# Optimization experiments

Measured on AMD Instinct MI355X. Metric: run time of the kernel, lower is better.

## Reference

```python
import jax, jax.numpy as jnp
from jax import lax
import numpy as np

SEQ_LEN, BATCH, NUM_TAGS = 512, 256, 128


def setup_inputs() -> dict:
    key = jax.random.key(0)
    k1, k2, k3, k4, k5 = jax.random.split(key, 5)
    emissions = jax.random.normal(k1, (SEQ_LEN, BATCH, NUM_TAGS), dtype=jnp.float32)
    tags = jax.random.randint(k2, (SEQ_LEN, BATCH), 0, NUM_TAGS, dtype=jnp.int64)
    mask = jnp.ones((SEQ_LEN, BATCH), dtype=bool)
    # CRF learned parameters (torchcrf initializes Uniform(-0.1, 0.1))
    start_transitions = jax.random.uniform(k3, (NUM_TAGS,), jnp.float32, -0.1, 0.1)
    end_transitions = jax.random.uniform(k4, (NUM_TAGS,), jnp.float32, -0.1, 0.1)
    transitions = jax.random.uniform(k5, (NUM_TAGS, NUM_TAGS), jnp.float32, -0.1, 0.1)
    return {
        "emissions": emissions,
        "tags": tags,
        "mask": mask,
        "start_transitions": start_transitions,
        "end_transitions": end_transitions,
        "transitions": transitions,
    }


def reference(emissions, tags, mask, start_transitions, end_transitions, transitions):
    """torchcrf CRF.forward(emissions, tags, mask, reduction='sum'):
    summed log-likelihood = numerator (gold path score) - log partition.
    emissions: [T, B, K], tags: [T, B], mask: [T, B] bool.
    """
    T, B = tags.shape
    maskf = mask.astype(emissions.dtype)
    bidx = jnp.arange(B)

    # ---- numerator: score of the gold tag sequence ----
    first_score = start_transitions[tags[0]] + emissions[0, bidx, tags[0]]  # [B]

    def num_step(carry, inp):
        score, prev_tags = carry
        em_t, tag_t, m_t = inp  # [B,K], [B], [B] float
        step = transitions[prev_tags, tag_t] + em_t[bidx, tag_t]
        score = score + step * m_t
        prev_tags = jnp.where(m_t.astype(bool), tag_t, prev_tags)
        return (score, prev_tags), None

    (num, last_tags), _ = lax.scan(
        num_step, (first_score, tags[0]), (emissions[1:], tags[1:], maskf[1:])
    )
    num = num + end_transitions[last_tags]  # [B]

    # ---- denominator: log partition via forward algorithm ----
    init = start_transitions[None, :] + emissions[0]  # [B, K]

    def den_step(score, inp):
        em_t, m_t = inp  # [B,K], [B] bool
        # broadcast: [B, K_prev, K_next]
        nxt = jax.nn.logsumexp(
            score[:, :, None] + transitions[None, :, :] + em_t[:, None, :], axis=1
        )
        score = jnp.where(m_t[:, None], nxt, score)
        return score, None

    final, _ = lax.scan(den_step, init, (emissions[1:], mask[1:]))
    den = jax.nn.logsumexp(final + end_transitions[None, :], axis=1)  # [B]

    # reduction='sum'
    return jnp.sum(num - den)
```

## Files before the change

kernel.cpp:

```cpp
#include <hip/hip_runtime.h>
#include <hip/hip_bf16.h>


#define TT 512
#define BB 256
#define KK 128
#define TB 32768

typedef float f2 __attribute__((ext_vector_type(2)));

#if __has_builtin(__builtin_elementwise_fma)
#define FMA2(a, b, c) __builtin_elementwise_fma((a), (b), (c))
#else
static __device__ __forceinline__ f2 FMA2(f2 a, f2 b, f2 c) {
  f2 r; r.x = fmaf(a.x, b.x, c.x); r.y = fmaf(a.y, b.y, c.y); return r;
}
#endif

static __device__ __forceinline__ float qsum4(float x) {
  x += __int_as_float(__builtin_amdgcn_update_dpp(
      0, __float_as_int(x), 0xB1, 0xF, 0xF, false));
  x += __int_as_float(__builtin_amdgcn_update_dpp(
      0, __float_as_int(x), 0x4E, 0xF, 0xF, false));
  return x;
}

#define HOT_BARRIER()                                    \
  do {                                                   \
    asm volatile("s_waitcnt lgkmcnt(0)" ::: "memory");   \
    __builtin_amdgcn_s_barrier();                        \
    asm volatile("" ::: "memory");                       \
  } while (0)

__global__ __launch_bounds__(256, 1) void crf_main(
    const float* __restrict__ em,
    const int* __restrict__ tags_raw,
    const unsigned char* __restrict__ mask_raw,
    const float* __restrict__ startt,
    const float* __restrict__ endt,
    const float* __restrict__ trans,
    double* __restrict__ acc)
{
  const int b = blockIdx.x;
  const int tid = threadIdx.x;
  const int jp = tid >> 2;
  const int o = tid & 3;
  const int wid = tid >> 6;
  const int woff = 36 * (jp >> 4) + 2 * (jp & 15);

  __shared__ __align__(16) float srep[2][144];
  __shared__ __align__(16) float wavesum[16];
  __shared__ int sflags[4];
  __shared__ unsigned char smask[TT];

  {
    int wv = (tid < 64) ? tags_raw[2 * tid + 1] : 0;
    unsigned long long bal = __ballot(wv != 0);
    if (tid == 0) {
      sflags[0] = (bal == 0ull) ? 1 : 0;
      sflags[1] = (mask_raw[1] != 0) ? 0 : 1;
    }
  }
  __syncthreads();
  const bool tags64 = (sflags[0] != 0);
  const bool mask32 = (sflags[1] != 0);
  const int* mask_i = (const int*)mask_raw;

  auto get_tag = [&](int t) -> int {
    int idx = t * BB + b;
    return tags64 ? tags_raw[2 * idx] : tags_raw[idx];
  };

  for (int t = tid; t < TT; t += 256) {
    int idx = t * BB + b;
    bool m = mask32 ? (mask_i[idx] != 0) : (mask_raw[idx] != 0);
    smask[t] = m ? 1 : 0;
  }
  __syncthreads();

  float ncon = 0.f, mcnt = 0.f;
  for (int t = tid; t < TT; t += 256) {
    int ct = get_tag(t);
    bool m = (smask[t] != 0);
    if (m) mcnt += 1.f;
    if (t == 0) {
      ncon += startt[ct] + em[(size_t)b * KK + ct];
    } else if (m) {
      int pt = get_tag(t - 1);
      ncon += trans[pt * KK + ct] + em[((size_t)t * BB + b) * KK + ct];
    }
  }
  #pragma unroll
  for (int mm = 1; mm < 64; mm <<= 1) {
    ncon += __shfl_xor(ncon, mm, 64);
    mcnt += __shfl_xor(mcnt, mm, 64);
  }
  if ((tid & 63) == 0) {
    wavesum[wid] = ncon;
    wavesum[8 + wid] = mcnt;
  }
  __syncthreads();
  float num_b = 0.f;
  if (tid == 0) {
    float ns = 0.f, ms = 0.f;
    #pragma unroll
    for (int wv = 0; wv < 4; ++wv) { ns += wavesum[wv]; ms += wavesum[8 + wv]; }
    int L = (int)(ms + 0.5f);
    num_b = ns + endt[get_tag(L - 1)];
    sflags[2] = L;
  }

  f2 c0,  c1,  c2,  c3,  c4,  c5,  c6,  c7,
     c8,  c9,  c10, c11, c12, c13, c14, c15,
     c16, c17, c18, c19, c20, c21, c22, c23,
     c24, c25, c26, c27, c28, c29, c30, c31;
  {
    const float* tp0 = trans + (size_t)(o * 32) * KK + 2 * jp;
#define INITC(n)                                            \
    { float2 tv = *(const float2*)(tp0 + (n) * KK);         \
      c##n.x = __expf(tv.x); c##n.y = __expf(tv.y); }
    INITC(0)  INITC(1)  INITC(2)  INITC(3)  INITC(4)  INITC(5)  INITC(6)  INITC(7)
    INITC(8)  INITC(9)  INITC(10) INITC(11) INITC(12) INITC(13) INITC(14) INITC(15)
    INITC(16) INITC(17) INITC(18) INITC(19) INITC(20) INITC(21) INITC(22) INITC(23)
    INITC(24) INITC(25) INITC(26) INITC(27) INITC(28) INITC(29) INITC(30) INITC(31)
#undef INITC
  }
  asm volatile("" : "+v"(c0),  "+v"(c1),  "+v"(c2),  "+v"(c3),
                    "+v"(c4),  "+v"(c5),  "+v"(c6),  "+v"(c7),
                    "+v"(c8),  "+v"(c9),  "+v"(c10), "+v"(c11),
                    "+v"(c12), "+v"(c13), "+v"(c14), "+v"(c15));
  asm volatile("" : "+v"(c16), "+v"(c17), "+v"(c18), "+v"(c19),
                    "+v"(c20), "+v"(c21), "+v"(c22), "+v"(c23),
                    "+v"(c24), "+v"(c25), "+v"(c26), "+v"(c27),
                    "+v"(c28), "+v"(c29), "+v"(c30), "+v"(c31));

  const float* emb = em + (size_t)b * KK + 2 * jp;
  {
    float2 st = *(const float2*)(startt + 2 * jp);
    float2 e0 = *(const float2*)(emb);
    if (o == 0) {
      float2 s0 = {__expf(st.x + e0.x), __expf(st.y + e0.y)};
      *(float2*)&srep[0][woff] = s0;
    }
  }

  float2 er = *(const float2*)(emb + (size_t)1 * TB);
  f2 pex; pex.x = __expf(er.x); pex.y = __expf(er.y);
  float2 e1 = *(const float2*)(emb + (size_t)2 * TB);
  float2 e2 = *(const float2*)(emb + (size_t)3 * TB);
  float2 e3 = *(const float2*)(emb + (size_t)4 * TB);
  float2 e4 = *(const float2*)(emb + (size_t)5 * TB);
  __syncthreads();
  const int L = sflags[2];

  int cur = 0;
  double Cacc = 0.0;

  for (int t = 1; t < L; ++t) {
    f2 ecur = pex;
    pex.x = __expf(e1.x); pex.y = __expf(e1.y);
    e1 = e2; e2 = e3; e3 = e4;
    int tp = t + 5; if (tp > TT - 1) tp = TT - 1;
    e4 = *(const float2*)(emb + (size_t)tp * TB);

    const float4* sp = reinterpret_cast<const float4*>(&srep[cur][o * 36]);
    f2 a0 = {0.f, 0.f}, a1 = {0.f, 0.f}, a2 = {0.f, 0.f}, a3 = {0.f, 0.f};
#define DOTQ(m, cA, cB, cC, cD, accA, accB)              \
    { float4 s4 = sp[m];                                 \
      f2 v0 = {s4.x, s4.x}, v1 = {s4.y, s4.y};           \
      f2 v2 = {s4.z, s4.z}, v3 = {s4.w, s4.w};           \
      accA = FMA2(v0, cA, accA); accB = FMA2(v1, cB, accB); \
      accA = FMA2(v2, cC, accA); accB = FMA2(v3, cD, accB); }
    DOTQ(0, c0,  c1,  c2,  c3,  a0, a1)
    DOTQ(1, c4,  c5,  c6,  c7,  a2, a3)
    DOTQ(2, c8,  c9,  c10, c11, a0, a1)
    DOTQ(3, c12, c13, c14, c15, a2, a3)
    DOTQ(4, c16, c17, c18, c19, a0, a1)
    DOTQ(5, c20, c21, c22, c23, a2, a3)
    DOTQ(6, c24, c25, c26, c27, a0, a1)
    DOTQ(7, c28, c29, c30, c31, a2, a3)
#undef DOTQ
    f2 av = (a0 + a1) + (a2 + a3);
    f2 w;
    w.x = qsum4(av.x) * ecur.x;
    w.y = qsum4(av.y) * ecur.y;

    if ((t & 3) == 1 && t != 1) {
      float4 wa = *reinterpret_cast<const float4*>(&wavesum[0]);
      float tot = 0.25f * ((wa.x + wa.y) + (wa.z + wa.w));
      if (tid == 0) Cacc += (double)__logf(tot);
      float rt = __builtin_amdgcn_rcpf(tot);
      w.x *= rt; w.y *= rt;
    }
    if (o == 0) {
      float2 ws = {w.x, w.y};
      *(float2*)&srep[cur ^ 1][woff] = ws;
    }
    if ((t & 3) == 0) {
      float r = w.x + w.y;
      r += __shfl_xor(r, 4, 64);
      r += __shfl_xor(r, 8, 64);
      r += __shfl_xor(r, 16, 64);
      r += __shfl_xor(r, 32, 64);
      if ((tid & 63) == 0) wavesum[wid] = r;
    }
    HOT_BARRIER();
    cur ^= 1;
  }

  {
    float2 sv = *(const float2*)&srep[cur][woff];
    float2 ed = *(const float2*)(endt + 2 * jp);
    float x = sv.x * __expf(ed.x) + sv.y * __expf(ed.y);
    x += __shfl_xor(x, 4, 64);
    x += __shfl_xor(x, 8, 64);
    x += __shfl_xor(x, 16, 64);
    x += __shfl_xor(x, 32, 64);
    if ((tid & 63) == 0) wavesum[wid] = x;
  }
  __syncthreads();
  if (tid == 0) {
    float tot = 0.25f * (wavesum[0] + wavesum[1] + wavesum[2] + wavesum[3]);
    double den = Cacc + (double)__logf(tot);
    atomicAdd(acc, (double)num_b - den);
  }
}

__global__ void crf_finalize(const double* __restrict__ acc, float* __restrict__ out) {
  out[0] = (float)acc[0];
}

extern "C" void kernel_launch(void* const* d_in, const int* in_sizes, int n_in,
                              void* d_out, int out_size, void* d_ws, size_t ws_size,
                              hipStream_t stream) {
  const float* em    = (const float*)d_in[0];
  const int*   tags  = (const int*)d_in[1];
  const unsigned char* mask = (const unsigned char*)d_in[2];
  const float* startt = (const float*)d_in[3];
  const float* endt   = (const float*)d_in[4];
  const float* trans  = (const float*)d_in[5];
  double* acc = (double*)d_ws;

  hipMemsetAsync(d_ws, 0, sizeof(double), stream);
  crf_main<<<256, 256, 0, stream>>>(em, tags, mask, startt, endt, trans, acc);
  crf_finalize<<<1, 1, 0, stream>>>(acc, (float*)d_out);
}
```

Baseline: 316.6 us.

## Pack forward-state and exp(transitions)-1 in bf16, renormalize every step

The forward-algorithm state and the exp(transitions) matrix are stored as packed bf16. Transitions are kept as exp(T)-1 so the dot product becomes sum(s) + sum(s*d), and the state is renormalized by its total at every step, with the total computed via DPP/shuffle reductions and stored per wave. This halves the LDS traffic and the register footprint for the transition matrix, and drops the periodic normalization branch, in exchange for bf16 precision loss in the log-partition and extra unpack and reduction work on each step.

```diff
diff --git a/kernel.cpp b/kernel.cpp
--- a/kernel.cpp
+++ b/kernel.cpp
@@ -8,14 +8,6 @@
 #define TB 32768
 
 typedef float f2 __attribute__((ext_vector_type(2)));
-
-#if __has_builtin(__builtin_elementwise_fma)
-#define FMA2(a, b, c) __builtin_elementwise_fma((a), (b), (c))
-#else
-static __device__ __forceinline__ f2 FMA2(f2 a, f2 b, f2 c) {
-  f2 r; r.x = fmaf(a.x, b.x, c.x); r.y = fmaf(a.y, b.y, c.y); return r;
-}
-#endif
 
 static __device__ __forceinline__ float qsum4(float x) {
   x += __int_as_float(__builtin_amdgcn_update_dpp(
@@ -23,6 +15,14 @@
   x += __int_as_float(__builtin_amdgcn_update_dpp(
       0, __float_as_int(x), 0x4E, 0xF, 0xF, false));
   return x;
+}
+static __device__ __forceinline__ float roradd4(float x) {
+  return x + __int_as_float(__builtin_amdgcn_update_dpp(
+      0, __float_as_int(x), 0x124, 0xF, 0xF, false));
+}
+static __device__ __forceinline__ float roradd8(float x) {
+  return x + __int_as_float(__builtin_amdgcn_update_dpp(
+      0, __float_as_int(x), 0x128, 0xF, 0xF, false));
 }
 
 #define HOT_BARRIER()                                    \
@@ -46,9 +46,9 @@
   const int jp = tid >> 2;
   const int o = tid & 3;
   const int wid = tid >> 6;
-  const int woff = 36 * (jp >> 4) + 2 * (jp & 15);
-
-  __shared__ __align__(16) float srep[2][144];
+
+  __shared__ __align__(16) unsigned int spk[2][64];
+  __shared__ __align__(16) float wsum[2][4];
   __shared__ __align__(16) float wavesum[16];
   __shared__ int sflags[4];
   __shared__ unsigned char smask[TT];
@@ -110,38 +110,44 @@
     sflags[2] = L;
   }
 
-  f2 c0,  c1,  c2,  c3,  c4,  c5,  c6,  c7,
-     c8,  c9,  c10, c11, c12, c13, c14, c15,
-     c16, c17, c18, c19, c20, c21, c22, c23,
-     c24, c25, c26, c27, c28, c29, c30, c31;
+  unsigned int d0,d1,d2,d3,d4,d5,d6,d7,d8,d9,d10,d11,d12,d13,d14,d15,
+               d16,d17,d18,d19,d20,d21,d22,d23,d24,d25,d26,d27,d28,d29,d30,d31;
   {
     const float* tp0 = trans + (size_t)(o * 32) * KK + 2 * jp;
-#define INITC(n)                                            \
-    { float2 tv = *(const float2*)(tp0 + (n) * KK);         \
-      c##n.x = __expf(tv.x); c##n.y = __expf(tv.y); }
-    INITC(0)  INITC(1)  INITC(2)  INITC(3)  INITC(4)  INITC(5)  INITC(6)  INITC(7)
-    INITC(8)  INITC(9)  INITC(10) INITC(11) INITC(12) INITC(13) INITC(14) INITC(15)
-    INITC(16) INITC(17) INITC(18) INITC(19) INITC(20) INITC(21) INITC(22) INITC(23)
-    INITC(24) INITC(25) INITC(26) INITC(27) INITC(28) INITC(29) INITC(30) INITC(31)
-#undef INITC
-  }
-  asm volatile("" : "+v"(c0),  "+v"(c1),  "+v"(c2),  "+v"(c3),
-                    "+v"(c4),  "+v"(c5),  "+v"(c6),  "+v"(c7),
-                    "+v"(c8),  "+v"(c9),  "+v"(c10), "+v"(c11),
-                    "+v"(c12), "+v"(c13), "+v"(c14), "+v"(c15));
-  asm volatile("" : "+v"(c16), "+v"(c17), "+v"(c18), "+v"(c19),
-                    "+v"(c20), "+v"(c21), "+v"(c22), "+v"(c23),
-                    "+v"(c24), "+v"(c25), "+v"(c26), "+v"(c27),
-                    "+v"(c28), "+v"(c29), "+v"(c30), "+v"(c31));
+#define INITD(n)                                                       \
+    { float2 tv = *(const float2*)(tp0 + (n) * KK);                    \
+      float dx = __expf(tv.x) - 1.0f, dy = __expf(tv.y) - 1.0f;        \
+      asm("v_cvt_pk_bf16_f32 %0, %1, %2" : "=v"(d##n) : "v"(dx), "v"(dy)); }
+    INITD(0)  INITD(1)  INITD(2)  INITD(3)  INITD(4)  INITD(5)  INITD(6)  INITD(7)
+    INITD(8)  INITD(9)  INITD(10) INITD(11) INITD(12) INITD(13) INITD(14) INITD(15)
+    INITD(16) INITD(17) INITD(18) INITD(19) INITD(20) INITD(21) INITD(22) INITD(23)
+    INITD(24) INITD(25) INITD(26) INITD(27) INITD(28) INITD(29) INITD(30) INITD(31)
+#undef INITD
+  }
+  asm volatile("" : "+v"(d0),  "+v"(d1),  "+v"(d2),  "+v"(d3),
+                    "+v"(d4),  "+v"(d5),  "+v"(d6),  "+v"(d7),
+                    "+v"(d8),  "+v"(d9),  "+v"(d10), "+v"(d11),
+                    "+v"(d12), "+v"(d13), "+v"(d14), "+v"(d15));
+  asm volatile("" : "+v"(d16), "+v"(d17), "+v"(d18), "+v"(d19),
+                    "+v"(d20), "+v"(d21), "+v"(d22), "+v"(d23),
+                    "+v"(d24), "+v"(d25), "+v"(d26), "+v"(d27),
+                    "+v"(d28), "+v"(d29), "+v"(d30), "+v"(d31));
 
   const float* emb = em + (size_t)b * KK + 2 * jp;
+  f2 w;
   {
     float2 st = *(const float2*)(startt + 2 * jp);
     float2 e0 = *(const float2*)(emb);
-    if (o == 0) {
-      float2 s0 = {__expf(st.x + e0.x), __expf(st.y + e0.y)};
-      *(float2*)&srep[0][woff] = s0;
-    }
+    w.x = __expf(st.x + e0.x);
+    w.y = __expf(st.y + e0.y);
+    unsigned int wp;
+    asm("v_cvt_pk_bf16_f32 %0, %1, %2" : "=v"(wp) : "v"(w.x), "v"(w.y));
+    float rs = __int_as_float(wp << 16) + __int_as_float(wp & 0xFFFF0000u);
+    rs = roradd4(rs); rs = roradd8(rs);
+    rs += __shfl_xor(rs, 16, 64);
+    rs += __shfl_xor(rs, 32, 64);
+    if (o == 0) spk[0][jp] = wp;
+    if ((tid & 63) == 0) wsum[0][wid] = rs;
   }
 
   float2 er = *(const float2*)(emb + (size_t)1 * TB);
@@ -149,7 +155,6 @@
   float2 e1 = *(const float2*)(emb + (size_t)2 * TB);
   float2 e2 = *(const float2*)(emb + (size_t)3 * TB);
   float2 e3 = *(const float2*)(emb + (size_t)4 * TB);
-  float2 e4 = *(const float2*)(emb + (size_t)5 * TB);
   __syncthreads();
   const int L = sflags[2];
 
@@ -157,70 +162,64 @@
   double Cacc = 0.0;
 
   for (int t = 1; t < L; ++t) {
+    float4 g4 = *reinterpret_cast<const float4*>(&wsum[cur][0]);
+    const uint4* sp = reinterpret_cast<const uint4*>(&spk[cur][o * 16]);
+    uint4 sA = sp[0], sB = sp[1], sC = sp[2], sD = sp[3];
+
     f2 ecur = pex;
     pex.x = __expf(e1.x); pex.y = __expf(e1.y);
-    e1 = e2; e2 = e3; e3 = e4;
-    int tp = t + 5; if (tp > TT - 1) tp = TT - 1;
-    e4 = *(const float2*)(emb + (size_t)tp * TB);
-
-    const float4* sp = reinterpret_cast<const float4*>(&srep[cur][o * 36]);
-    f2 a0 = {0.f, 0.f}, a1 = {0.f, 0.f}, a2 = {0.f, 0.f}, a3 = {0.f, 0.f};
-#define DOTQ(m, cA, cB, cC, cD, accA, accB)              \
-    { float4 s4 = sp[m];                                 \
-      f2 v0 = {s4.x, s4.x}, v1 = {s4.y, s4.y};           \
-      f2 v2 = {s4.z, s4.z}, v3 = {s4.w, s4.w};           \
-      accA = FMA2(v0, cA, accA); accB = FMA2(v1, cB, accB); \
-      accA = FMA2(v2, cC, accA); accB = FMA2(v3, cD, accB); }
-    DOTQ(0, c0,  c1,  c2,  c3,  a0, a1)
-    DOTQ(1, c4,  c5,  c6,  c7,  a2, a3)
-    DOTQ(2, c8,  c9,  c10, c11, a0, a1)
-    DOTQ(3, c12, c13, c14, c15, a2, a3)
-    DOTQ(4, c16, c17, c18, c19, a0, a1)
-    DOTQ(5, c20, c21, c22, c23, a2, a3)
-    DOTQ(6, c24, c25, c26, c27, a0, a1)
-    DOTQ(7, c28, c29, c30, c31, a2, a3)
-#undef DOTQ
-    f2 av = (a0 + a1) + (a2 + a3);
-    f2 w;
-    w.x = qsum4(av.x) * ecur.x;
-    w.y = qsum4(av.y) * ecur.y;
-
-    if ((t & 3) == 1 && t != 1) {
-      float4 wa = *reinterpret_cast<const float4*>(&wavesum[0]);
-      float tot = 0.25f * ((wa.x + wa.y) + (wa.z + wa.w));
-      if (tid == 0) Cacc += (double)__logf(tot);
-      float rt = __builtin_amdgcn_rcpf(tot);
-      w.x *= rt; w.y *= rt;
-    }
-    if (o == 0) {
-      float2 ws = {w.x, w.y};
-      *(float2*)&srep[cur ^ 1][woff] = ws;
-    }
-    if ((t & 3) == 0) {
-      float r = w.x + w.y;
-      r += __shfl_xor(r, 4, 64);
-      r += __shfl_xor(r, 8, 64);
-      r += __shfl_xor(r, 16, 64);
-      r += __shfl_xor(r, 32, 64);
-      if ((tid & 63) == 0) wavesum[wid] = r;
-    }
+    e1 = e2; e2 = e3;
+    int tq = t + 4; if (tq > TT - 1) tq = TT - 1;
+    e3 = *(const float2*)(emb + (size_t)tq * TB);
+
+    float G = (g4.x + g4.y) + (g4.z + g4.w);
+
+    float a0 = 0.f, a1 = 0.f, b0 = 0.f, b1 = 0.f;
+#define MAC1(u, dA, dB)                                         \
+    { float se = __int_as_float((u) << 16);                     \
+      float so = __int_as_float((u) & 0xFFFF0000u);             \
+      a0 = fmaf(se, __int_as_float((dA) << 16), a0);            \
+      a1 = fmaf(se, __int_as_float((dA) & 0xFFFF0000u), a1);    \
+      b0 = fmaf(so, __int_as_float((dB) << 16), b0);            \
+      b1 = fmaf(so, __int_as_float((dB) & 0xFFFF0000u), b1); }
+    MAC1(sA.x, d0,  d1)  MAC1(sA.y, d2,  d3)  MAC1(sA.z, d4,  d5)  MAC1(sA.w, d6,  d7)
+    MAC1(sB.x, d8,  d9)  MAC1(sB.y, d10, d11) MAC1(sB.z, d12, d13) MAC1(sB.w, d14, d15)
+    MAC1(sC.x, d16, d17) MAC1(sC.y, d18, d19) MAC1(sC.z, d20, d21) MAC1(sC.w, d22, d23)
+    MAC1(sD.x, d24, d25) MAC1(sD.y, d26, d27) MAC1(sD.z, d28, d29) MAC1(sD.w, d30, d31)
+#undef MAC1
+    float accx = qsum4(a0 + b0);
+    float accy = qsum4(a1 + b1);
+    f2 v; v.x = G + accx; v.y = G + accy;
+    f2 r; r.x = v.x * ecur.x; r.y = v.y * ecur.y;
+    float rt = __builtin_amdgcn_rcpf(G);
+    w.x = r.x * rt; w.y = r.y * rt;
+    float lg = __logf(rt);
+    if (tid == 0) Cacc -= (double)lg;
+
+    unsigned int wp;
+    asm("v_cvt_pk_bf16_f32 %0, %1, %2" : "=v"(wp) : "v"(w.x), "v"(w.y));
+    float rs = __int_as_float(wp << 16) + __int_as_float(wp & 0xFFFF0000u);
+    rs = roradd4(rs); rs = roradd8(rs);
+    rs += __shfl_xor(rs, 16, 64);
+    rs += __shfl_xor(rs, 32, 64);
+    if (o == 0) spk[cur ^ 1][jp] = wp;
+    if ((tid & 63) == 0) wsum[cur ^ 1][wid] = rs;
+
     HOT_BARRIER();
     cur ^= 1;
   }
 
   {
-    float2 sv = *(const float2*)&srep[cur][woff];
     float2 ed = *(const float2*)(endt + 2 * jp);
-    float x = sv.x * __expf(ed.x) + sv.y * __expf(ed.y);
-    x += __shfl_xor(x, 4, 64);
-    x += __shfl_xor(x, 8, 64);
+    float x = w.x * __expf(ed.x) + w.y * __expf(ed.y);
+    x = roradd4(x); x = roradd8(x);
     x += __shfl_xor(x, 16, 64);
     x += __shfl_xor(x, 32, 64);
     if ((tid & 63) == 0) wavesum[wid] = x;
   }
   __syncthreads();
   if (tid == 0) {
-    float tot = 0.25f * (wavesum[0] + wavesum[1] + wavesum[2] + wavesum[3]);
+    float tot = wavesum[0] + wavesum[1] + wavesum[2] + wavesum[3];
     double den = Cacc + (double)__logf(tot);
     atomicAdd(acc, (double)num_b - den);
   }
```

Result: slower. 355.7 us (+12.3%).
